# Kernel tuning notes

Measured on AMD Instinct MI355X. Metric: run time of the kernel, lower is better.

Reference implementation:

```python
import jax, jax.numpy as jnp
from jax import lax
import numpy as np

SEL = [46, 92]
A_SEL = [16, 32]
EPS = 1e-16


def _descriptors(xyz, atomtypes, box):
    # xyz: (B,N,3) float, atomtypes: (B,N) int, box: scalar
    B, N, _ = xyz.shape
    dm = xyz[:, :, None, :] - xyz[:, None, :, :] + EPS          # (B,N,N,3)
    dm = dm - box * jnp.round(dm / box)                          # min-image PBC
    dist = jnp.sqrt(jnp.sum(dm * dm, axis=-1))                   # (B,N,N)
    self_mask = jnp.eye(N, dtype=bool)[None]                     # exclude self
    radial, a_xyz_list, a_dist_list = [], [], []
    lf_d = lf_i = None
    for j, (selj, aselj) in enumerate(zip(SEL, A_SEL)):
        mask = (atomtypes == j)[:, None, :] & (~self_mask)       # (B,N,N)
        d_j = jnp.where(mask, dist, jnp.inf)
        k = max(selj, aselj, 2)
        neg, idx = lax.top_k(-d_j, k)                            # k smallest
        sd = -neg                                                # (B,N,k)
        if j == 0:
            lf_d, lf_i = sd[..., :2], idx[..., :2]
        else:
            better = sd[..., :2] < lf_d
            lf_d = jnp.where(better, sd[..., :2], lf_d)
            lf_i = jnp.where(better, idx[..., :2], lf_i)
        radial.append(1.0 / (sd[..., :selj] + EPS))
        a_xyz_list.append(jnp.take_along_axis(dm, idx[..., :aselj, None], axis=2))
        a_dist_list.append(sd[..., :aselj])
    a_xyz = jnp.concatenate(a_xyz_list, axis=2)                  # (B,N,sumA,3)
    a_dist = jnp.concatenate(a_dist_list, axis=2)[..., None]     # (B,N,sumA,1)
    # local frame from the 2 globally nearest neighbors
    l_xyz = jnp.take_along_axis(dm, lf_i[..., None], axis=2) / (lf_d[..., None] + EPS)
    r0, r1 = l_xyz[:, :, 0], l_xyz[:, :, 1]                      # (B,N,3)
    v2 = r1 - jnp.sum(r0 * r1, -1, keepdims=True) * r0
    v2 = v2 / jnp.linalg.norm(v2, axis=-1, keepdims=True)
    v3 = jnp.cross(r0, r1)
    v3 = v3 / jnp.linalg.norm(v3, axis=-1, keepdims=True)
    A = jnp.stack([r0, v2, v3], axis=-2)                         # (B,N,3,3)
    a_xyz = a_xyz / (a_dist + EPS)
    a_xyz = jnp.einsum('bnij,bnkj->bnki', A, a_xyz)
    a_xyz = a_xyz / (a_dist + EPS)  # faithful: source divides by a_dist twice
    return jnp.concatenate(radial + [a_xyz.reshape(B, N, -1)], axis=-1)


def _energy(xyz, atomtypes, box, params):
    # norm is (mean=0, std=1) in the source -> identity, skipped.
    desc = _descriptors(xyz, atomtypes, box)
    e = jnp.zeros(desc.shape[:2], desc.dtype)
    for t, layers in enumerate(params):
        h = desc
        for (W, b) in layers[:-1]:
            h = jnp.tanh(h @ W + b)
        W, b = layers[-1]
        e = jnp.where(atomtypes == t, (h @ W + b)[..., 0], e)
    return jnp.sum(e, axis=1)                                    # (B,)


def setup_inputs():
    key = jax.random.key(0)
    ks = jax.random.split(key, 16)
    B, N, box = 2, 2048, 27
    xyz = jax.random.uniform(ks[0], (B, N, 3), dtype=jnp.float32) * box
    atomtypes = jax.random.randint(ks[1], (B, N), 0, 2)
    D = sum(SEL) + 3 * sum(A_SEL)  # 282
    sizes = [D, 64, 64, 1]
    inp = {'xyz': xyz, 'atomtypes': atomtypes, 'box_size': box}
    ki = 2
    for t in range(2):
        for l in range(3):
            fi, fo = sizes[l], sizes[l + 1]
            inp[f'W{t}_{l}'] = jax.random.normal(ks[ki], (fi, fo), dtype=jnp.float32) / np.sqrt(fi).astype(np.float32)
            inp[f'b{t}_{l}'] = jnp.zeros((fo,), jnp.float32)
            ki += 1
    return inp


def reference(xyz, atomtypes, box_size, W0_0, b0_0, W0_1, b0_1, W0_2, b0_2,
              W1_0, b1_0, W1_1, b1_1, W1_2, b1_2):
    params = [[(W0_0, b0_0), (W0_1, b0_1), (W0_2, b0_2)],
              [(W1_0, b1_0), (W1_1, b1_1), (W1_2, b1_2)]]
    energy = _energy(xyz, atomtypes, box_size, params)
    forces = -jax.grad(lambda x: jnp.sum(_energy(x, atomtypes, box_size, params)))(xyz)
    return energy, forces
```

## Files before the change

### kernel.cpp

```cpp
#include <hip/hip_runtime.h>
#include <stdint.h>
#include <math.h>

#define BLOCK 256
#define WPB 4
#define SEL0 46
#define SEL1 92
#define ASEL0 16
#define ASEL1 32
#define NNB 138
#define NANG 48
#define DDIM 282
#define HID 64
#define FEPS 1e-16f
#define NPT 32
#define CAP 128
#define NREP 16

__device__ __forceinline__ float mimg(float dx, float box, float ibox) {
    return dx - box * rintf(dx * ibox);
}

__device__ __forceinline__ void wsync() {
    asm volatile("s_waitcnt lgkmcnt(0)" ::: "memory");
    __builtin_amdgcn_wave_barrier();
}

__device__ __forceinline__ void decode(unsigned long long k, float& d, int& j) {
    uint32_t idx = (uint32_t)(k & 0xFFFFFFFFull);
    if (idx == 0xFFFFFFFFu) { d = 1e30f; j = -1; }
    else { d = __uint_as_float((uint32_t)(k >> 32)); j = (int)idx; }
}

__global__ __launch_bounds__(BLOCK)
void reduce_kernel(const float* __restrict__ rep, float* __restrict__ out,
                   int total, int Bc, int eoff, int rstride, int nrep)
{
    int e = blockIdx.x * BLOCK + threadIdx.x;
    if (e >= total) return;
    int src = (e < Bc) ? (eoff + e) : (e - Bc);
    float s = 0.0f;
    for (int r = 0; r < nrep; ++r) s += rep[(size_t)r * rstride + src];
    out[e] = s;
}

__global__ __launch_bounds__(BLOCK, 4)
void md_kernel(const float* __restrict__ xyz, const int* __restrict__ types,
               const void* __restrict__ boxp,
               const float* __restrict__ W0a, const float* __restrict__ B0a,
               const float* __restrict__ W1a, const float* __restrict__ B1a,
               const float* __restrict__ W2a, const float* __restrict__ B2a,
               const float* __restrict__ W0b, const float* __restrict__ B0b,
               const float* __restrict__ W1b, const float* __restrict__ B1b,
               const float* __restrict__ W2b, const float* __restrict__ B2b,
               float* __restrict__ out, float* __restrict__ repbase,
               int nrep, int eoff, int rstride, int B, int N)
{
    __shared__ unsigned long long A0s[WPB][CAP];
    __shared__ unsigned long long A1s[WPB][CAP];
    __shared__ float sdescs[WPB][DDIM];
    __shared__ float sgs[WPB][DDIM];
    __shared__ float sAs[WPB][9];
    __shared__ float sh1s[WPB][HID];
    __shared__ float sdh2s[WPB][HID];
    __shared__ float sdh1s[WPB][HID];

    const int w = threadIdx.x >> 6;
    const int lane = threadIdx.x & 63;
    const int atom = blockIdx.x * WPB + w;
    if (atom >= B * N) return;
    const int b = atom / N;
    const int i = atom - b * N;

    unsigned long long* A0w = A0s[w];
    unsigned long long* A1w = A1s[w];
    float* sdescw = sdescs[w];
    float* sgw = sgs[w];
    float* sAw = sAs[w];
    float* sh1w = sh1s[w];
    float* sdh2w = sdh2s[w];
    float* sdh1w = sdh1s[w];

    float* Fout;
    float* Eout;
    if (repbase) {
        float* base = repbase + (size_t)(atom % nrep) * rstride;
        Fout = base; Eout = base + eoff;
    } else {
        Fout = out + B; Eout = out;
    }

    int ib_test = ((const int*)boxp)[0];
    float box = (ib_test > 0 && ib_test < 1000000) ? (float)ib_test
                                                   : ((const float*)boxp)[0];
    float ibox = 1.0f / box;

    const float* X = xyz + (size_t)b * N * 3;
    const int*   T = types + (size_t)b * N;
    const int ti = T[i];
    const float xi = X[3*i+0], yi = X[3*i+1], zi = X[3*i+2];

    uint32_t rk[NPT];
    #pragma unroll
    for (int jj = 0; jj < NPT; ++jj) {
        int j = jj * 64 + lane;
        uint32_t k = 0x7FFFFFFFu;
        if (j < N && j != i) {
            float dx = mimg(xi - X[3*j+0], box, ibox);
            float dy = mimg(yi - X[3*j+1], box, ibox);
            float dz = mimg(zi - X[3*j+2], box, ibox);
            float d = sqrtf(dx*dx + dy*dy + dz*dz);
            k = __float_as_uint(d) | (T[j] ? 0x80000000u : 0u);
        }
        rk[jj] = k;
    }

    uint32_t t1 = 0;
    #pragma unroll
    for (int jj = 0; jj < NPT; ++jj) t1 += (rk[jj] >> 31);
    #pragma unroll
    for (int o = 32; o > 0; o >>= 1) t1 += __shfl_down(t1, o, 64);
    t1 = __shfl(t1, 0, 64);
    const int tot1 = (int)t1;
    const int tot0 = (N - 1) - tot1;
    const int need0 = min(SEL0, tot0);
    const int need1 = min(SEL1, tot1);

    const float vol = box * box * box;
    const float c43pi = 4.18879020f;
    float R0 = cbrtf(0.5f * (need0 + CAP) * vol / (c43pi * fmaxf((float)tot0, 1.0f)));
    float R1 = cbrtf(0.5f * (need1 + CAP) * vol / (c43pi * fmaxf((float)tot1, 1.0f)));
    uint32_t Rb0 = __float_as_uint(R0), Rb1 = __float_as_uint(R1);
    float lo0 = 0.0f, hi0 = -1.0f, lo1 = 0.0f, hi1 = -1.0f;
    for (int it = 0; it < 20; ++it) {
        uint32_t c0 = 0, c1 = 0;
        #pragma unroll
        for (int jj = 0; jj < NPT; ++jj) {
            uint32_t k = rk[jj];
            c0 += ((k < 0x80000000u) && (k < Rb0));
            c1 += ((k >= 0x80000000u) && ((k & 0x7FFFFFFFu) < Rb1));
        }
        uint32_t packed = c0 | (c1 << 16);
        #pragma unroll
        for (int o = 32; o > 0; o >>= 1) packed += __shfl_down(packed, o, 64);
        packed = __shfl(packed, 0, 64);
        int cc0 = (int)(packed & 0xFFFFu);
        int cc1 = (int)(packed >> 16);
        bool done0 = (cc0 >= need0 && cc0 <= CAP);
        bool done1 = (cc1 >= need1 && cc1 <= CAP);
        if (done0 && done1) break;
        if (!done0) {
            if (cc0 < need0) { lo0 = R0; R0 = (hi0 > 0.0f) ? 0.5f*(lo0+hi0) : R0*1.3f; }
            else             { hi0 = R0; R0 = 0.5f*(lo0+hi0); }
            Rb0 = __float_as_uint(R0);
        }
        if (!done1) {
            if (cc1 < need1) { lo1 = R1; R1 = (hi1 > 0.0f) ? 0.5f*(lo1+hi1) : R1*1.3f; }
            else             { hi1 = R1; R1 = 0.5f*(lo1+hi1); }
            Rb1 = __float_as_uint(R1);
        }
    }

    const unsigned long long lmlt = (1ull << lane) - 1ull;
    int base0 = 0, base1 = 0;
    #pragma unroll
    for (int jj = 0; jj < NPT; ++jj) {
        uint32_t k = rk[jj];
        bool p0 = (k < 0x80000000u) && (k < Rb0);
        bool p1 = (k >= 0x80000000u) && ((k & 0x7FFFFFFFu) < Rb1);
        unsigned long long m0 = __ballot(p0);
        unsigned long long m1 = __ballot(p1);
        if (p0) {
            int pos = base0 + __popcll(m0 & lmlt);
            if (pos < CAP)
                A0w[pos] = ((unsigned long long)k << 32) | (uint32_t)(jj*64 + lane);
        }
        if (p1) {
            int pos = base1 + __popcll(m1 & lmlt);
            if (pos < CAP)
                A1w[pos] = ((unsigned long long)(k & 0x7FFFFFFFu) << 32) | (uint32_t)(jj*64 + lane);
        }
        base0 += __popcll(m0);
        base1 += __popcll(m1);
    }
    const int c0n = min(base0, CAP);
    const int c1n = min(base1, CAP);
    #pragma unroll
    for (int t = lane; t < CAP; t += 64) {
        if (t >= c0n) A0w[t] = ~0ull;
        if (t >= c1n) A1w[t] = ~0ull;
    }
    wsync();

    {
        unsigned long long va = A0w[lane], vb = A0w[lane + 64];
        unsigned long long wa = A1w[lane], wb = A1w[lane + 64];
        #pragma unroll
        for (int size = 2; size <= 128; size <<= 1) {
            #pragma unroll
            for (int stride = 64; stride > 0; stride >>= 1) {
                if (stride >= size) continue;
                if (stride == 64) {
                    unsigned long long mn = va < vb ? va : vb;
                    unsigned long long mx = va < vb ? vb : va;
                    va = mn; vb = mx;
                    mn = wa < wb ? wa : wb;
                    mx = wa < wb ? wb : wa;
                    wa = mn; wb = mx;
                } else {
                    bool keep_lo = (lane & stride) == 0;
                    bool asc0 = ((lane & size) == 0);
                    bool asc1 = (((lane + 64) & size) == 0);
                    unsigned long long oa = __shfl_xor(va, stride, 64);
                    unsigned long long ob = __shfl_xor(vb, stride, 64);
                    va = (asc0 == keep_lo) ? (va < oa ? va : oa) : (va > oa ? va : oa);
                    vb = (asc1 == keep_lo) ? (vb < ob ? vb : ob) : (vb > ob ? vb : ob);
                    oa = __shfl_xor(wa, stride, 64);
                    ob = __shfl_xor(wb, stride, 64);
                    wa = (asc0 == keep_lo) ? (wa < oa ? wa : oa) : (wa > oa ? wa : oa);
                    wb = (asc1 == keep_lo) ? (wb < ob ? wb : ob) : (wb > ob ? wb : ob);
                }
            }
        }
        A0w[lane] = va; A0w[lane + 64] = vb;
        A1w[lane] = wa; A1w[lane + 64] = wb;
    }
    wsync();

    for (int t = lane; t < NNB; t += 64) {
        unsigned long long k = (t < SEL0) ? A0w[t] : A1w[t - SEL0];
        float d; int j; decode(k, d, j);
        sdescw[t] = 1.0f / (d + FEPS);
    }

    float f_ld0 = 1.0f, f_ld1 = 1.0f; int f_j0 = -1, f_j1 = -1;
    float r0x=0,r0y=0,r0z=0, r1x=0,r1y=0,r1z=0;
    float u0x=0,u0y=0,u0z=0, u1x=0,u1y=0,u1z=0;
    float f_s=0, f_n2=1, f_n3=1;
    float e2x=0,e2y=0,e2z=0, e3x=0,e3y=0,e3z=0;
    if (lane == 0) {
        float da0, da1, db0, db1; int ja0, ja1, jb0, jb1;
        decode(A0w[0], da0, ja0);
        decode(A0w[1], da1, ja1);
        decode(A1w[0], db0, jb0);
        decode(A1w[1], db1, jb1);
        f_ld0 = (db0 < da0) ? db0 : da0;  f_j0 = (db0 < da0) ? jb0 : ja0;
        f_ld1 = (db1 < da1) ? db1 : da1;  f_j1 = (db1 < da1) ? jb1 : ja1;
        if (f_j0 < 0) f_j0 = i;
        if (f_j1 < 0) f_j1 = i;
        u0x = mimg(xi - X[3*f_j0+0], box, ibox);
        u0y = mimg(yi - X[3*f_j0+1], box, ibox);
        u0z = mimg(zi - X[3*f_j0+2], box, ibox);
        u1x = mimg(xi - X[3*f_j1+0], box, ibox);
        u1y = mimg(yi - X[3*f_j1+1], box, ibox);
        u1z = mimg(zi - X[3*f_j1+2], box, ibox);
        float id0 = 1.0f/(f_ld0 + FEPS), id1 = 1.0f/(f_ld1 + FEPS);
        r0x = u0x*id0; r0y = u0y*id0; r0z = u0z*id0;
        r1x = u1x*id1; r1y = u1y*id1; r1z = u1z*id1;
        f_s = r0x*r1x + r0y*r1y + r0z*r1z;
        float v2x = r1x - f_s*r0x, v2y = r1y - f_s*r0y, v2z = r1z - f_s*r0z;
        f_n2 = sqrtf(v2x*v2x + v2y*v2y + v2z*v2z);
        e2x = v2x/f_n2; e2y = v2y/f_n2; e2z = v2z/f_n2;
        float cx = r0y*r1z - r0z*r1y;
        float cy = r0z*r1x - r0x*r1z;
        float cz = r0x*r1y - r0y*r1x;
        f_n3 = sqrtf(cx*cx + cy*cy + cz*cz);
        e3x = cx/f_n3; e3y = cy/f_n3; e3z = cz/f_n3;
        sAw[0]=r0x; sAw[1]=r0y; sAw[2]=r0z;
        sAw[3]=e2x; sAw[4]=e2y; sAw[5]=e2z;
        sAw[6]=e3x; sAw[7]=e3y; sAw[8]=e3z;
    }
    wsync();

    if (lane < NANG) {
        int slot = (lane < ASEL0) ? lane : SEL0 + (lane - ASEL0);
        unsigned long long k = (slot < SEL0) ? A0w[slot] : A1w[slot - SEL0];
        float d; int j; decode(k, d, j);
        float dx = 0, dy = 0, dz = 0;
        if (j >= 0) {
            dx = mimg(xi - X[3*j+0], box, ibox);
            dy = mimg(yi - X[3*j+1], box, ibox);
            dz = mimg(zi - X[3*j+2], box, ibox);
        }
        float de = d + FEPS;
        float q = 1.0f/(de*de);
        float wx = sAw[0]*dx + sAw[1]*dy + sAw[2]*dz;
        float wy = sAw[3]*dx + sAw[4]*dy + sAw[5]*dz;
        float wz = sAw[6]*dx + sAw[7]*dy + sAw[8]*dz;
        sdescw[NNB + 3*lane + 0] = wx*q;
        sdescw[NNB + 3*lane + 1] = wy*q;
        sdescw[NNB + 3*lane + 2] = wz*q;
    }
    wsync();

    const float* W0 = ti ? W0b : W0a;  const float* B0 = ti ? B0b : B0a;
    const float* W1 = ti ? W1b : W1a;  const float* B1 = ti ? B1b : B1a;
    const float* W2 = ti ? W2b : W2a;  const float* B2 = ti ? B2b : B2a;

    float acc = B0[lane];
    for (int d = 0; d < DDIM; ++d) acc = fmaf(sdescw[d], W0[d*HID + lane], acc);
    float h1 = tanhf(acc);
    sh1w[lane] = h1;
    wsync();

    float acc2 = B1[lane];
    #pragma unroll
    for (int m = 0; m < HID; ++m) acc2 = fmaf(sh1w[m], W1[m*HID + lane], acc2);
    float h2 = tanhf(acc2);
    float w2v = W2[lane];
    float part = h2 * w2v;
    #pragma unroll
    for (int o = 32; o > 0; o >>= 1) part += __shfl_down(part, o, 64);
    if (lane == 0) atomicAdd(&Eout[b], part + B2[0]);
    float dh2 = (1.0f - h2*h2) * w2v;
    sdh2w[lane] = dh2;
    wsync();

    float accb = 0.0f;
    #pragma unroll
    for (int m = 0; m < HID; ++m) accb = fmaf(W1[lane*HID + m], sdh2w[m], accb);
    float dh1 = (1.0f - h1*h1) * accb;
    sdh1w[lane] = dh1;
    wsync();

    for (int d = lane; d < DDIM; d += 64) {
        float a = 0.0f;
        #pragma unroll
        for (int m = 0; m < HID; ++m) a = fmaf(W0[d*HID + m], sdh1w[m], a);
        sgw[d] = a;
    }
    wsync();

    float rG[9];
    #pragma unroll
    for (int q9 = 0; q9 < 9; ++q9) rG[q9] = 0.0f;
    float fix = 0.0f, fiy = 0.0f, fiz = 0.0f;

    for (int t = lane; t < NNB; t += 64) {
        unsigned long long k = (t < SEL0) ? A0w[t] : A1w[t - SEL0];
        float d; int j; decode(k, d, j);
        if (j >= 0) {
            float dx = mimg(xi - X[3*j+0], box, ibox);
            float dy = mimg(yi - X[3*j+1], box, ibox);
            float dz = mimg(zi - X[3*j+2], box, ibox);
            float gr = sgw[t];
            float de = d + FEPS;
            float coef = -gr / (d * de * de);
            float gx = coef*dx, gy = coef*dy, gz = coef*dz;
            int a = -1;
            if (t < ASEL0) a = t;
            else if (t >= SEL0 && t < SEL0 + ASEL1) a = ASEL0 + (t - SEL0);
            if (a >= 0) {
                float q = 1.0f/(de*de);
                float gax = sgw[NNB+3*a+0], gay = sgw[NNB+3*a+1], gaz = sgw[NNB+3*a+2];
                float wx = sAw[0]*dx + sAw[1]*dy + sAw[2]*dz;
                float wy = sAw[3]*dx + sAw[4]*dy + sAw[5]*dz;
                float wz = sAw[6]*dx + sAw[7]*dy + sAw[8]*dz;
                float tx = sAw[0]*gax + sAw[3]*gay + sAw[6]*gaz;
                float ty = sAw[1]*gax + sAw[4]*gay + sAw[7]*gaz;
                float tz = sAw[2]*gax + sAw[5]*gay + sAw[8]*gaz;
                float gw = gax*wx + gay*wy + gaz*wz;
                float c2 = -2.0f * gw * q / (de * d);
                gx += q*tx + c2*dx;
                gy += q*ty + c2*dy;
                gz += q*tz + c2*dz;
                rG[0] += gax*dx*q; rG[1] += gax*dy*q; rG[2] += gax*dz*q;
                rG[3] += gay*dx*q; rG[4] += gay*dy*q; rG[5] += gay*dz*q;
                rG[6] += gaz*dx*q; rG[7] += gaz*dy*q; rG[8] += gaz*dz*q;
            }
            float* Fj = Fout + 3*((size_t)b*N + j);
            atomicAdd(&Fj[0], gx); atomicAdd(&Fj[1], gy); atomicAdd(&Fj[2], gz);
            fix -= gx; fiy -= gy; fiz -= gz;
        }
    }

    #pragma unroll
    for (int o = 32; o > 0; o >>= 1) {
        #pragma unroll
        for (int q9 = 0; q9 < 9; ++q9) rG[q9] += __shfl_down(rG[q9], o, 64);
        fix += __shfl_down(fix, o, 64);
        fiy += __shfl_down(fiy, o, 64);
        fiz += __shfl_down(fiz, o, 64);
    }

    if (lane == 0) {
        float g0x=rG[0], g0y=rG[1], g0z=rG[2];
        float g2x=rG[3], g2y=rG[4], g2z=rG[5];
        float g3x=rG[6], g3y=rG[7], g3z=rG[8];
        float d3 = g3x*e3x + g3y*e3y + g3z*e3z;
        float in3 = 1.0f/f_n3;
        float dcx = (g3x - d3*e3x)*in3;
        float dcy = (g3y - d3*e3y)*in3;
        float dcz = (g3z - d3*e3z)*in3;
        float gr0x = r1y*dcz - r1z*dcy;
        float gr0y = r1z*dcx - r1x*dcz;
        float gr0z = r1x*dcy - r1y*dcx;
        float gr1x = dcy*r0z - dcz*r0y;
        float gr1y = dcz*r0x - dcx*r0z;
        float gr1z = dcx*r0y - dcy*r0x;
        float d2 = g2x*e2x + g2y*e2y + g2z*e2z;
        float in2 = 1.0f/f_n2;
        float dvx = (g2x - d2*e2x)*in2;
        float dvy = (g2y - d2*e2y)*in2;
        float dvz = (g2z - d2*e2z)*in2;
        gr1x += dvx; gr1y += dvy; gr1z += dvz;
        gr0x -= f_s*dvx; gr0y -= f_s*dvy; gr0z -= f_s*dvz;
        float dss = -(dvx*r0x + dvy*r0y + dvz*r0z);
        gr0x += dss*r1x; gr0y += dss*r1y; gr0z += dss*r1z;
        gr1x += dss*r0x; gr1y += dss*r0y; gr1z += dss*r0z;
        gr0x += g0x; gr0y += g0y; gr0z += g0z;
        float de0 = f_ld0 + FEPS;
        float dot0 = gr0x*u0x + gr0y*u0y + gr0z*u0z;
        float k0 = dot0 / (f_ld0 * de0 * de0);
        float gu0x = gr0x/de0 - k0*u0x;
        float gu0y = gr0y/de0 - k0*u0y;
        float gu0z = gr0z/de0 - k0*u0z;
        float de1 = f_ld1 + FEPS;
        float dot1 = gr1x*u1x + gr1y*u1y + gr1z*u1z;
        float k1 = dot1 / (f_ld1 * de1 * de1);
        float gu1x = gr1x/de1 - k1*u1x;
        float gu1y = gr1y/de1 - k1*u1y;
        float gu1z = gr1z/de1 - k1*u1z;
        float* Fj0 = Fout + 3*((size_t)b*N + f_j0);
        atomicAdd(&Fj0[0], gu0x); atomicAdd(&Fj0[1], gu0y); atomicAdd(&Fj0[2], gu0z);
        float* Fj1 = Fout + 3*((size_t)b*N + f_j1);
        atomicAdd(&Fj1[0], gu1x); atomicAdd(&Fj1[1], gu1y); atomicAdd(&Fj1[2], gu1z);
        fix -= gu0x + gu1x;
        fiy -= gu0y + gu1y;
        fiz -= gu0z + gu1z;
        float* Fi = Fout + 3*((size_t)b*N + i);
        atomicAdd(&Fi[0], fix); atomicAdd(&Fi[1], fiy); atomicAdd(&Fi[2], fiz);
    }
}

extern "C" void kernel_launch(void* const* d_in, const int* in_sizes, int n_in,
                              void* d_out, int out_size, void* d_ws, size_t ws_size,
                              hipStream_t stream) {
    const float* xyz  = (const float*)d_in[0];
    const int*   types = (const int*)d_in[1];
    const void*  boxp = d_in[2];
    int BN = in_sizes[1];
    int B = out_size - 3*BN;
    if (B < 1) B = 1;
    int N = BN / B;

    int eoff = ((3 * BN + 31) / 32) * 32;
    int rstride = eoff + ((B + 31) / 32) * 32;
    int nrep = NREP;
    size_t need = (size_t)nrep * rstride * sizeof(float);
    if (need > ws_size) {
        nrep = (int)(ws_size / ((size_t)rstride * sizeof(float)));
        if (nrep > NREP) nrep = NREP;
    }
    float* rep = (nrep >= 1) ? (float*)d_ws : nullptr;

    if (rep) {
        hipMemsetAsync(d_ws, 0, (size_t)nrep * rstride * sizeof(float), stream);
    } else {
        hipMemsetAsync(d_out, 0, (size_t)out_size * sizeof(float), stream);
    }

    int nblk = (BN + WPB - 1) / WPB;
    md_kernel<<<dim3(nblk), dim3(BLOCK), 0, stream>>>(
        xyz, types, boxp,
        (const float*)d_in[3],  (const float*)d_in[4],
        (const float*)d_in[5],  (const float*)d_in[6],
        (const float*)d_in[7],  (const float*)d_in[8],
        (const float*)d_in[9],  (const float*)d_in[10],
        (const float*)d_in[11], (const float*)d_in[12],
        (const float*)d_in[13], (const float*)d_in[14],
        (float*)d_out, rep, nrep > 0 ? nrep : 1, eoff, rstride, B, N);

    if (rep) {
        int total = out_size;
        int nb = (total + BLOCK - 1) / BLOCK;
        reduce_kernel<<<dim3(nb), dim3(BLOCK), 0, stream>>>(
            rep, (float*)d_out, total, B, eoff, rstride, nrep);
    }
}
```

Before: 274.5 us.

## Coalesce transposed backward matvecs via LDS tiles and fuse radius search with compaction

Rewrites the backward transposed matrix-vector products (W1^T·dh2 and W0^T·dh1) so lanes read weight rows coalesced. Each product is staged in a padded shared-memory tile and reduced with shuffles, replacing the old strided per-lane row reads. The radius bisection now does compaction directly with ballots each iteration, removing the separate count pass and shuffle reductions. The type count uses ballot/popcount, and the forward layer-0 dot product is split into four independent accumulators for ILP. The cost is extra LDS per block, more wave syncs, and LDS writes on every bisection iteration.

```diff
diff --git a/kernel.cpp b/kernel.cpp
--- a/kernel.cpp
+++ b/kernel.cpp
@@ -30,6 +30,32 @@
     uint32_t idx = (uint32_t)(k & 0xFFFFFFFFull);
     if (idx == 0xFFFFFFFFu) { d = 1e30f; j = -1; }
     else { d = __uint_as_float((uint32_t)(k >> 32)); j = (int)idx; }
+}
+
+__device__ __forceinline__ void matvec_T(const float* __restrict__ M, int nrows,
+                                         float vreg, float* __restrict__ outw,
+                                         float (*tile)[65], int lane)
+{
+    const int dl = lane & 15, mc = lane >> 4;
+    for (int r0 = 0; r0 < nrows; r0 += 16) {
+        const int rows = (nrows - r0 < 16) ? (nrows - r0) : 16;
+        if (rows == 16) {
+            #pragma unroll
+            for (int k = 0; k < 16; ++k)
+                tile[k][lane] = M[(r0 + k) * HID + lane] * vreg;
+        } else {
+            for (int k = 0; k < rows; ++k)
+                tile[k][lane] = M[(r0 + k) * HID + lane] * vreg;
+        }
+        wsync();
+        float s = 0.0f;
+        #pragma unroll
+        for (int mm = 0; mm < 16; ++mm) s += tile[dl][mc * 16 + mm];
+        s += __shfl_xor(s, 16, 64);
+        s += __shfl_xor(s, 32, 64);
+        if (lane < rows) outw[r0 + lane] = s;
+        wsync();
+    }
 }
 
 __global__ __launch_bounds__(BLOCK)
@@ -62,8 +88,8 @@
     __shared__ float sgs[WPB][DDIM];
     __shared__ float sAs[WPB][9];
     __shared__ float sh1s[WPB][HID];
-    __shared__ float sdh2s[WPB][HID];
     __shared__ float sdh1s[WPB][HID];
+    __shared__ float tiles[WPB][16][65];
 
     const int w = threadIdx.x >> 6;
     const int lane = threadIdx.x & 63;
@@ -78,8 +104,8 @@
     float* sgw = sgs[w];
     float* sAw = sAs[w];
     float* sh1w = sh1s[w];
-    float* sdh2w = sdh2s[w];
     float* sdh1w = sdh1s[w];
+    float (*tile)[65] = tiles[w];
 
     float* Fout;
     float* Eout;
@@ -117,10 +143,8 @@
 
     uint32_t t1 = 0;
     #pragma unroll
-    for (int jj = 0; jj < NPT; ++jj) t1 += (rk[jj] >> 31);
-    #pragma unroll
-    for (int o = 32; o > 0; o >>= 1) t1 += __shfl_down(t1, o, 64);
-    t1 = __shfl(t1, 0, 64);
+    for (int jj = 0; jj < NPT; ++jj)
+        t1 += (uint32_t)__popcll(__ballot((rk[jj] >> 31) != 0u));
     const int tot1 = (int)t1;
     const int tot0 = (N - 1) - tot1;
     const int need0 = min(SEL0, tot0);
@@ -130,61 +154,46 @@
     const float c43pi = 4.18879020f;
     float R0 = cbrtf(0.5f * (need0 + CAP) * vol / (c43pi * fmaxf((float)tot0, 1.0f)));
     float R1 = cbrtf(0.5f * (need1 + CAP) * vol / (c43pi * fmaxf((float)tot1, 1.0f)));
-    uint32_t Rb0 = __float_as_uint(R0), Rb1 = __float_as_uint(R1);
     float lo0 = 0.0f, hi0 = -1.0f, lo1 = 0.0f, hi1 = -1.0f;
+    const unsigned long long lmlt = (1ull << lane) - 1ull;
+    int c0n = 0, c1n = 0;
     for (int it = 0; it < 20; ++it) {
-        uint32_t c0 = 0, c1 = 0;
+        uint32_t Rb0 = __float_as_uint(R0), Rb1 = __float_as_uint(R1);
+        int base0 = 0, base1 = 0;
         #pragma unroll
         for (int jj = 0; jj < NPT; ++jj) {
             uint32_t k = rk[jj];
-            c0 += ((k < 0x80000000u) && (k < Rb0));
-            c1 += ((k >= 0x80000000u) && ((k & 0x7FFFFFFFu) < Rb1));
-        }
-        uint32_t packed = c0 | (c1 << 16);
-        #pragma unroll
-        for (int o = 32; o > 0; o >>= 1) packed += __shfl_down(packed, o, 64);
-        packed = __shfl(packed, 0, 64);
-        int cc0 = (int)(packed & 0xFFFFu);
-        int cc1 = (int)(packed >> 16);
-        bool done0 = (cc0 >= need0 && cc0 <= CAP);
-        bool done1 = (cc1 >= need1 && cc1 <= CAP);
-        if (done0 && done1) break;
-        if (!done0) {
-            if (cc0 < need0) { lo0 = R0; R0 = (hi0 > 0.0f) ? 0.5f*(lo0+hi0) : R0*1.3f; }
-            else             { hi0 = R0; R0 = 0.5f*(lo0+hi0); }
-            Rb0 = __float_as_uint(R0);
-        }
-        if (!done1) {
-            if (cc1 < need1) { lo1 = R1; R1 = (hi1 > 0.0f) ? 0.5f*(lo1+hi1) : R1*1.3f; }
-            else             { hi1 = R1; R1 = 0.5f*(lo1+hi1); }
-            Rb1 = __float_as_uint(R1);
-        }
-    }
-
-    const unsigned long long lmlt = (1ull << lane) - 1ull;
-    int base0 = 0, base1 = 0;
-    #pragma unroll
-    for (int jj = 0; jj < NPT; ++jj) {
-        uint32_t k = rk[jj];
-        bool p0 = (k < 0x80000000u) && (k < Rb0);
-        bool p1 = (k >= 0x80000000u) && ((k & 0x7FFFFFFFu) < Rb1);
-        unsigned long long m0 = __ballot(p0);
-        unsigned long long m1 = __ballot(p1);
-        if (p0) {
-            int pos = base0 + __popcll(m0 & lmlt);
-            if (pos < CAP)
-                A0w[pos] = ((unsigned long long)k << 32) | (uint32_t)(jj*64 + lane);
-        }
-        if (p1) {
-            int pos = base1 + __popcll(m1 & lmlt);
-            if (pos < CAP)
-                A1w[pos] = ((unsigned long long)(k & 0x7FFFFFFFu) << 32) | (uint32_t)(jj*64 + lane);
-        }
-        base0 += __popcll(m0);
-        base1 += __popcll(m1);
-    }
-    const int c0n = min(base0, CAP);
-    const int c1n = min(base1, CAP);
+            bool p0 = (k < 0x80000000u) && (k < Rb0);
+            bool p1 = (k >= 0x80000000u) && ((k & 0x7FFFFFFFu) < Rb1);
+            unsigned long long m0 = __ballot(p0);
+            unsigned long long m1 = __ballot(p1);
+            if (p0) {
+                int pos = base0 + __popcll(m0 & lmlt);
+                if (pos < CAP)
+                    A0w[pos] = ((unsigned long long)k << 32) | (uint32_t)(jj*64 + lane);
+            }
+            if (p1) {
+                int pos = base1 + __popcll(m1 & lmlt);
+                if (pos < CAP)
+                    A1w[pos] = ((unsigned long long)(k & 0x7FFFFFFFu) << 32) | (uint32_t)(jj*64 + lane);
+            }
+            base0 += __popcll(m0);
+            base1 += __popcll(m1);
+        }
+        bool ok0 = (base0 >= need0 && base0 <= CAP);
+        bool ok1 = (base1 >= need1 && base1 <= CAP);
+        c0n = min(base0, CAP);
+        c1n = min(base1, CAP);
+        if (ok0 && ok1) break;
+        if (!ok0) {
+            if (base0 < need0) { lo0 = R0; R0 = (hi0 > 0.0f) ? 0.5f*(lo0+hi0) : R0*1.3f; }
+            else               { hi0 = R0; R0 = 0.5f*(lo0+hi0); }
+        }
+        if (!ok1) {
+            if (base1 < need1) { lo1 = R1; R1 = (hi1 > 0.0f) ? 0.5f*(lo1+hi1) : R1*1.3f; }
+            else               { hi1 = R1; R1 = 0.5f*(lo1+hi1); }
+        }
+    }
     #pragma unroll
     for (int t = lane; t < CAP; t += 64) {
         if (t >= c0n) A0w[t] = ~0ull;
@@ -297,9 +306,16 @@
     const float* W1 = ti ? W1b : W1a;  const float* B1 = ti ? B1b : B1a;
     const float* W2 = ti ? W2b : W2a;  const float* B2 = ti ? B2b : B2a;
 
-    float acc = B0[lane];
-    for (int d = 0; d < DDIM; ++d) acc = fmaf(sdescw[d], W0[d*HID + lane], acc);
-    float h1 = tanhf(acc);
+    float a0 = 0.0f, a1 = 0.0f, a2 = 0.0f, a3 = 0.0f;
+    for (int d = 0; d < DDIM - 2; d += 4) {
+        a0 = fmaf(sdescw[d+0], W0[(d+0)*HID + lane], a0);
+        a1 = fmaf(sdescw[d+1], W0[(d+1)*HID + lane], a1);
+        a2 = fmaf(sdescw[d+2], W0[(d+2)*HID + lane], a2);
+        a3 = fmaf(sdescw[d+3], W0[(d+3)*HID + lane], a3);
+    }
+    a0 = fmaf(sdescw[DDIM-2], W0[(DDIM-2)*HID + lane], a0);
+    a1 = fmaf(sdescw[DDIM-1], W0[(DDIM-1)*HID + lane], a1);
+    float h1 = tanhf(B0[lane] + ((a0 + a1) + (a2 + a3)));
     sh1w[lane] = h1;
     wsync();
 
@@ -313,23 +329,11 @@
     for (int o = 32; o > 0; o >>= 1) part += __shfl_down(part, o, 64);
     if (lane == 0) atomicAdd(&Eout[b], part + B2[0]);
     float dh2 = (1.0f - h2*h2) * w2v;
-    sdh2w[lane] = dh2;
-    wsync();
-
-    float accb = 0.0f;
-    #pragma unroll
-    for (int m = 0; m < HID; ++m) accb = fmaf(W1[lane*HID + m], sdh2w[m], accb);
-    float dh1 = (1.0f - h1*h1) * accb;
-    sdh1w[lane] = dh1;
-    wsync();
-
-    for (int d = lane; d < DDIM; d += 64) {
-        float a = 0.0f;
-        #pragma unroll
-        for (int m = 0; m < HID; ++m) a = fmaf(W0[d*HID + m], sdh1w[m], a);
-        sgw[d] = a;
-    }
-    wsync();
+
+    matvec_T(W1, HID, dh2, sdh1w, tile, lane);
+    float dh1 = (1.0f - h1*h1) * sdh1w[lane];
+
+    matvec_T(W0, DDIM, dh1, sgw, tile, lane);
 
     float rG[9];
     #pragma unroll
```

Result: slower. 323.8 us (+17.9%).

## Route force atomics to per-XCD replica buffers with workgroup-scope atomics

Applied to the files above, without the earlier changes.

Each block now picks its replica buffer from the hardware XCC id plus the block parity, so all writes to a replica come from a single XCD. Force and energy atomics then use workgroup-scope relaxed adds, intended to be resolved in the XCD-local L2 instead of going to device-coherent memory. This relies on workgroup scope being sufficient for cross-CU adds within one XCD and on the reduce kernel running afterward. The change also drops the dh2 shared array by reusing the dh1 buffer with an extra wave sync.

```diff
diff --git a/kernel.cpp b/kernel.cpp
--- a/kernel.cpp
+++ b/kernel.cpp
@@ -30,6 +30,12 @@
     uint32_t idx = (uint32_t)(k & 0xFFFFFFFFull);
     if (idx == 0xFFFFFFFFu) { d = 1e30f; j = -1; }
     else { d = __uint_as_float((uint32_t)(k >> 32)); j = (int)idx; }
+}
+
+__device__ __forceinline__ void atomF(float* p, float v, bool wg) {
+    if (wg) (void)__hip_atomic_fetch_add(p, v, __ATOMIC_RELAXED,
+                                         __HIP_MEMORY_SCOPE_WORKGROUP);
+    else    atomicAdd(p, v);
 }
 
 __global__ __launch_bounds__(BLOCK)
@@ -62,7 +68,6 @@
     __shared__ float sgs[WPB][DDIM];
     __shared__ float sAs[WPB][9];
     __shared__ float sh1s[WPB][HID];
-    __shared__ float sdh2s[WPB][HID];
     __shared__ float sdh1s[WPB][HID];
 
     const int w = threadIdx.x >> 6;
@@ -78,13 +83,16 @@
     float* sgw = sgs[w];
     float* sAw = sAs[w];
     float* sh1w = sh1s[w];
-    float* sdh2w = sdh2s[w];
     float* sdh1w = sdh1s[w];
 
+    const bool wg = (repbase != nullptr);
     float* Fout;
     float* Eout;
-    if (repbase) {
-        float* base = repbase + (size_t)(atom % nrep) * rstride;
+    if (wg) {
+        uint32_t xcc;
+        asm volatile("s_getreg_b32 %0, hwreg(HW_REG_XCC_ID)" : "=s"(xcc));
+        int ridx = (int)((xcc & 7u) * 2u + (blockIdx.x & 1u));
+        float* base = repbase + (size_t)ridx * rstride;
         Fout = base; Eout = base + eoff;
     } else {
         Fout = out + B; Eout = out;
@@ -311,14 +319,15 @@
     float part = h2 * w2v;
     #pragma unroll
     for (int o = 32; o > 0; o >>= 1) part += __shfl_down(part, o, 64);
-    if (lane == 0) atomicAdd(&Eout[b], part + B2[0]);
+    if (lane == 0) atomF(&Eout[b], part + B2[0], wg);
     float dh2 = (1.0f - h2*h2) * w2v;
-    sdh2w[lane] = dh2;
+    sdh1w[lane] = dh2;
     wsync();
 
     float accb = 0.0f;
     #pragma unroll
-    for (int m = 0; m < HID; ++m) accb = fmaf(W1[lane*HID + m], sdh2w[m], accb);
+    for (int m = 0; m < HID; ++m) accb = fmaf(W1[lane*HID + m], sdh1w[m], accb);
+    wsync();
     float dh1 = (1.0f - h1*h1) * accb;
     sdh1w[lane] = dh1;
     wsync();
@@ -369,7 +378,7 @@
                 rG[6] += gaz*dx*q; rG[7] += gaz*dy*q; rG[8] += gaz*dz*q;
             }
             float* Fj = Fout + 3*((size_t)b*N + j);
-            atomicAdd(&Fj[0], gx); atomicAdd(&Fj[1], gy); atomicAdd(&Fj[2], gz);
+            atomF(&Fj[0], gx, wg); atomF(&Fj[1], gy, wg); atomF(&Fj[2], gz, wg);
             fix -= gx; fiy -= gy; fiz -= gz;
         }
     }
@@ -422,14 +431,14 @@
         float gu1y = gr1y/de1 - k1*u1y;
         float gu1z = gr1z/de1 - k1*u1z;
         float* Fj0 = Fout + 3*((size_t)b*N + f_j0);
-        atomicAdd(&Fj0[0], gu0x); atomicAdd(&Fj0[1], gu0y); atomicAdd(&Fj0[2], gu0z);
+        atomF(&Fj0[0], gu0x, wg); atomF(&Fj0[1], gu0y, wg); atomF(&Fj0[2], gu0z, wg);
         float* Fj1 = Fout + 3*((size_t)b*N + f_j1);
-        atomicAdd(&Fj1[0], gu1x); atomicAdd(&Fj1[1], gu1y); atomicAdd(&Fj1[2], gu1z);
+        atomF(&Fj1[0], gu1x, wg); atomF(&Fj1[1], gu1y, wg); atomF(&Fj1[2], gu1z, wg);
         fix -= gu0x + gu1x;
         fiy -= gu0y + gu1y;
         fiz -= gu0z + gu1z;
         float* Fi = Fout + 3*((size_t)b*N + i);
-        atomicAdd(&Fi[0], fix); atomicAdd(&Fi[1], fiy); atomicAdd(&Fi[2], fiz);
+        atomF(&Fi[0], fix, wg); atomF(&Fi[1], fiy, wg); atomF(&Fi[2], fiz, wg);
     }
 }
 
@@ -448,15 +457,12 @@
     int rstride = eoff + ((B + 31) / 32) * 32;
     int nrep = NREP;
     size_t need = (size_t)nrep * rstride * sizeof(float);
-    if (need > ws_size) {
-        nrep = (int)(ws_size / ((size_t)rstride * sizeof(float)));
-        if (nrep > NREP) nrep = NREP;
-    }
-    float* rep = (nrep >= 1) ? (float*)d_ws : nullptr;
+    float* rep = (need <= ws_size) ? (float*)d_ws : nullptr;
 
     if (rep) {
-        hipMemsetAsync(d_ws, 0, (size_t)nrep * rstride * sizeof(float), stream);
+        hipMemsetAsync(d_ws, 0, need, stream);
     } else {
+        nrep = 1;
         hipMemsetAsync(d_out, 0, (size_t)out_size * sizeof(float), stream);
     }
 
@@ -469,7 +475,7 @@
         (const float*)d_in[9],  (const float*)d_in[10],
         (const float*)d_in[11], (const float*)d_in[12],
         (const float*)d_in[13], (const float*)d_in[14],
-        (float*)d_out, rep, nrep > 0 ? nrep : 1, eoff, rstride, B, N);
+        (float*)d_out, rep, nrep, eoff, rstride, B, N);
 
     if (rep) {
         int total = out_size;
```

After: 282.7 us. +3.0%, slower.
